# Kernel optimization log

Hardware: AMD Instinct MI355X
Metric: run time of the kernel (lower is better)

## Reference

```python
import jax, jax.numpy as jnp
import numpy as np

T, B, FEAT = 256, 512, 8
HID = 256
IN_DIM = 4  # QCNN output dim


def _linear_params(key, out_dim, in_dim, scale=0.1):
    kw, kb = jax.random.split(key)
    W = jax.random.normal(kw, (out_dim, in_dim), dtype=jnp.float32) * scale
    b = jax.random.normal(kb, (out_dim,), dtype=jnp.float32) * scale
    return W, b


def setup_inputs() -> dict:
    key = jax.random.key(0)
    ks = jax.random.split(key, 12)
    inputs = jax.random.normal(ks[0], (T, B, FEAT), dtype=jnp.float32)
    # QCNN feature extractor linears (torch Linear: W is [out, in])
    fm_w, fm_b = _linear_params(ks[1], 16, FEAT)
    c1_w, c1_b = _linear_params(ks[2], 16, 16)
    p1_w, p1_b = _linear_params(ks[3], 12, 16)
    c2_w, c2_b = _linear_params(ks[4], 8, 12)
    p2_w, p2_b = _linear_params(ks[5], 4, 8)
    c3_w, c3_b = _linear_params(ks[6], 4, 4)
    # LSTM gate linears: (IN_DIM + HID) -> HID
    f_w, f_b = _linear_params(ks[7], HID, IN_DIM + HID)
    i_w, i_b = _linear_params(ks[8], HID, IN_DIM + HID)
    u_w, u_b = _linear_params(ks[9], HID, IN_DIM + HID)
    o_w, o_b = _linear_params(ks[10], HID, IN_DIM + HID)
    # tagger head: HID -> 1
    head_w, head_b = _linear_params(ks[11], 1, HID)
    return dict(inputs=inputs, fm_w=fm_w, fm_b=fm_b, c1_w=c1_w, c1_b=c1_b,
                p1_w=p1_w, p1_b=p1_b, c2_w=c2_w, c2_b=c2_b, p2_w=p2_w, p2_b=p2_b,
                c3_w=c3_w, c3_b=c3_b, f_w=f_w, f_b=f_b, i_w=i_w, i_b=i_b,
                u_w=u_w, u_b=u_b, o_w=o_w, o_b=o_b, head_w=head_w, head_b=head_b)


def _lin(x, W, b):
    return x @ W.T + b


def reference(inputs, fm_w, fm_b, c1_w, c1_b, p1_w, p1_b, c2_w, c2_b,
              p2_w, p2_b, c3_w, c3_b, f_w, f_b, i_w, i_b, u_w, u_b,
              o_w, o_b, head_w, head_b):
    seq_len, batch, _ = inputs.shape
    # QCNN feature extractor has no cross-timestep dependency -> apply to all steps at once
    x = jnp.tanh(_lin(inputs, fm_w, fm_b))
    x = jnp.tanh(_lin(x, c1_w, c1_b))
    x = jnp.tanh(_lin(x, p1_w, p1_b))
    x = jnp.tanh(_lin(x, c2_w, c2_b))
    x = jnp.tanh(_lin(x, p2_w, p2_b))
    feats = jnp.tanh(_lin(x, c3_w, c3_b))  # [T, B, 4]

    h0 = jnp.zeros((batch, HID), dtype=inputs.dtype)
    c0 = jnp.zeros((batch, HID), dtype=inputs.dtype)

    def step(carry, xt):
        hx, cx = carry
        combined = jnp.concatenate([xt, hx], axis=1)  # [B, 4+HID]
        f = jax.nn.sigmoid(_lin(combined, f_w, f_b))
        i = jax.nn.sigmoid(_lin(combined, i_w, i_b))
        g = jnp.tanh(_lin(combined, u_w, u_b))
        o = jax.nn.sigmoid(_lin(combined, o_w, o_b))
        cx = f * cx + i * g
        hx = o * jnp.tanh(cx)
        return (hx, cx), hx

    (_, _), lstm_out = jax.lax.scan(step, (h0, c0), feats)  # [T, B, HID]
    out = _lin(lstm_out, head_w, head_b)  # [T, B, 1]
    return out
```

## Files before the change

kernel.cpp:

```cpp
#include <hip/hip_runtime.h>
#include <hip/hip_bf16.h>
#include <hip/hip_fp16.h>
#include <stdint.h>

#define T_STEPS 256
#define BATCH 512

typedef _Float16 f16x8 __attribute__((ext_vector_type(8)));
typedef _Float16 h2_t  __attribute__((ext_vector_type(2)));
typedef float    f32x4 __attribute__((ext_vector_type(4)));

__device__ __forceinline__ float fdot2(uint32_t w, uint32_t c, float acc) {
#if __has_builtin(__builtin_amdgcn_fdot2)
    h2_t a, b;
    __builtin_memcpy(&a, &w, 4);
    __builtin_memcpy(&b, &c, 4);
    return __builtin_amdgcn_fdot2(a, b, acc, false);
#else
    union { uint32_t u; _Float16 h[2]; } A, B;
    A.u = w; B.u = c;
    return acc + (float)A.h[0]*(float)B.h[0] + (float)A.h[1]*(float)B.h[1];
#endif
}

__device__ __forceinline__ float sigmoidf_(float x) {
    return 1.f / (1.f + __expf(-x));
}
__device__ __forceinline__ float tanhf_(float x) {
    float ax = fabsf(x);
    float e = __expf(-2.f * ax);
    float r = (1.f - e) / (1.f + e);
    return copysignf(r, x);
}

__device__ __forceinline__ float sel4(int d, float a, float b, float c, float e) {
    float lo = (d & 1) ? b : a;
    float hi = (d & 1) ? e : c;
    return (d & 2) ? hi : lo;
}

#define MFMA_AG(c, aa, bb) \
    asm volatile("v_mfma_f32_16x16x32_f16 %0, %1, %2, %0" : "+v"(c) : "v"(aa), "a"(bb))

__global__ void concat_qw(const float* __restrict__ fm_w, const float* __restrict__ fm_b,
                          const float* __restrict__ c1_w, const float* __restrict__ c1_b,
                          const float* __restrict__ p1_w, const float* __restrict__ p1_b,
                          const float* __restrict__ c2_w, const float* __restrict__ c2_b,
                          const float* __restrict__ p2_w, const float* __restrict__ p2_b,
                          const float* __restrict__ c3_w, const float* __restrict__ c3_b,
                          float* __restrict__ qw) {
    for (int k = threadIdx.x; k < 780; k += 256) {
        float v;
        if      (k < 128) v = fm_w[k];
        else if (k < 144) v = fm_b[k-128];
        else if (k < 400) v = c1_w[k-144];
        else if (k < 416) v = c1_b[k-400];
        else if (k < 608) v = p1_w[k-416];
        else if (k < 620) v = p1_b[k-608];
        else if (k < 716) v = c2_w[k-620];
        else if (k < 724) v = c2_b[k-716];
        else if (k < 756) v = p2_w[k-724];
        else if (k < 760) v = p2_b[k-756];
        else if (k < 776) v = c3_w[k-760];
        else              v = c3_b[k-776];
        qw[k] = v;
    }
}

__global__ void pack_bfrag(const float* __restrict__ f_w, const float* __restrict__ i_w,
                           const float* __restrict__ u_w, const float* __restrict__ o_w,
                           uint4* __restrict__ bfragsG) {
    int idx = blockIdx.x * 256 + threadIdx.x;
    int l = idx & 63, q = (idx >> 6) & 7, n = idx >> 9;
    int col = n * 16 + (l & 15);
    int g = col >> 8, j = col & 255;
    const float* W = (g == 0) ? f_w : (g == 1) ? i_w : (g == 2) ? u_w : o_w;
    union { uint4 u; _Float16 h[8]; } P;
#pragma unroll
    for (int e = 0; e < 8; ++e) {
        int k = q * 32 + ((l >> 4) * 8) + e;
        P.h[e] = (_Float16)W[j * 260 + 4 + k];
    }
    bfragsG[idx] = P.u;
}

__global__ void pack_xw(const float* __restrict__ f_w, const float* __restrict__ i_w,
                        const float* __restrict__ u_w, const float* __restrict__ o_w,
                        _Float16* __restrict__ xwG) {
    int t = blockIdx.x * 256 + threadIdx.x;
    int g = t >> 10, k = (t >> 8) & 3, j = t & 255;
    const float* W = (g == 0) ? f_w : (g == 1) ? i_w : (g == 2) ? u_w : o_w;
    xwG[t] = (_Float16)W[j * 260 + k];
}

__global__ void qcnn_kernel(const float* __restrict__ in, const float* __restrict__ qw,
                            _Float16* __restrict__ feats) {
    int r = blockIdx.x * 256 + threadIdx.x;
    const float* x = in + (size_t)r * 8;
    float v0[8];
#pragma unroll
    for (int i = 0; i < 8; ++i) v0[i] = x[i];
    float v1[16];
#pragma unroll
    for (int o = 0; o < 16; ++o) {
        float s = qw[128 + o];
#pragma unroll
        for (int i = 0; i < 8; ++i) s += qw[o*8 + i] * v0[i];
        v1[o] = tanhf_(s);
    }
    float v2[16];
#pragma unroll
    for (int o = 0; o < 16; ++o) {
        float s = qw[400 + o];
#pragma unroll
        for (int i = 0; i < 16; ++i) s += qw[144 + o*16 + i] * v1[i];
        v2[o] = tanhf_(s);
    }
    float v3[12];
#pragma unroll
    for (int o = 0; o < 12; ++o) {
        float s = qw[608 + o];
#pragma unroll
        for (int i = 0; i < 16; ++i) s += qw[416 + o*16 + i] * v2[i];
        v3[o] = tanhf_(s);
    }
    float v4[8];
#pragma unroll
    for (int o = 0; o < 8; ++o) {
        float s = qw[716 + o];
#pragma unroll
        for (int i = 0; i < 12; ++i) s += qw[620 + o*12 + i] * v3[i];
        v4[o] = tanhf_(s);
    }
    float v5[4];
#pragma unroll
    for (int o = 0; o < 4; ++o) {
        float s = qw[756 + o];
#pragma unroll
        for (int i = 0; i < 8; ++i) s += qw[724 + o*8 + i] * v4[i];
        v5[o] = tanhf_(s);
    }
    union { uint32_t u[2]; _Float16 h[4]; } P;
#pragma unroll
    for (int o = 0; o < 4; ++o) {
        float s = qw[776 + o];
#pragma unroll
        for (int i = 0; i < 4; ++i) s += qw[760 + o*4 + i] * v5[i];
        P.h[o] = (_Float16)tanhf_(s);
    }
    *reinterpret_cast<uint2*>(feats + (size_t)r * 4) = make_uint2(P.u[0], P.u[1]);
}

__global__ __launch_bounds__(256, 1)
void lstm_kernel(const uint4* __restrict__ bfragsG, const _Float16* __restrict__ xwG,
                 const _Float16* __restrict__ feats,
                 const float* __restrict__ f_b, const float* __restrict__ i_b,
                 const float* __restrict__ u_b, const float* __restrict__ o_b,
                 const float* __restrict__ head_w, const float* __restrict__ head_bp,
                 float* __restrict__ out) {
    __shared__ uint4     blds45[2][64][64];
    __shared__ uint4     blds6o[16][64];
    __shared__ __align__(16) _Float16 comb[2][2][256];
    __shared__ float     redL[2][4][2];

    const int tid = threadIdx.x;
    const int w   = tid >> 6;
    const int l   = tid & 63;
    const int d_  = l >> 4;
    const int jl  = (w * 4 + d_) * 16 + (l & 15);
    const int s0  = blockIdx.x * 2;

    for (int idx = tid; idx < 8192; idx += 256) {
        int n = idx >> 7, qq = (idx >> 6) & 1, ll = idx & 63;
        blds45[qq][n][ll] = bfragsG[(n * 8 + 4 + qq) * 64 + ll];
    }
    for (int idx = tid; idx < 1024; idx += 256) {
        int nn = idx >> 6, ll = idx & 63;
        blds6o[nn][ll] = bfragsG[((48 + nn) * 8 + 6) * 64 + ll];
    }
    reinterpret_cast<uint32_t*>(&comb[0][0][0])[tid] = 0u;

    f16x8 Br[16][4];
#pragma unroll
    for (int m = 0; m < 16; ++m) {
        const int n = (m >> 2) * 16 + w * 4 + (m & 3);
#pragma unroll
        for (int q = 0; q < 4; ++q) {
            Br[m][q] = *reinterpret_cast<const f16x8*>(bfragsG + (n * 8 + q) * 64 + l);
            asm volatile("" : "+a"(Br[m][q]));
        }
    }

    float bias_[4] = { f_b[jl], i_b[jl], u_b[jl], o_b[jl] };
    uint32_t xwp0[4], xwp1[4];
#pragma unroll
    for (int g = 0; g < 4; ++g) {
        union { uint32_t u; _Float16 h[2]; } P;
        P.h[0] = xwG[g*1024 +       jl]; P.h[1] = xwG[g*1024 + 256 + jl];
        xwp0[g] = P.u;
        P.h[0] = xwG[g*1024 + 512 + jl]; P.h[1] = xwG[g*1024 + 768 + jl];
        xwp1[g] = P.u;
    }
    const float hwj = head_w[jl];
    const float hb  = head_bp[0];
    uint2 xr0 = *reinterpret_cast<const uint2*>(feats + ((size_t)0 * BATCH + s0    ) * 4);
    uint2 xr1 = *reinterpret_cast<const uint2*>(feats + ((size_t)0 * BATCH + s0 + 1) * 4);

    __syncthreads();

    float cs0 = 0.f, cs1 = 0.f;

#pragma unroll 1
    for (int t = 0; t < T_STEPS; ++t) {
        const int cur = t & 1;
        uint2 xn0 = xr0, xn1 = xr1;
        if (t + 1 < T_STEPS) {
            xn0 = *reinterpret_cast<const uint2*>(feats + ((size_t)(t+1) * BATCH + s0    ) * 4);
            xn1 = *reinterpret_cast<const uint2*>(feats + ((size_t)(t+1) * BATCH + s0 + 1) * 4);
        }

        const _Float16* ab = &comb[cur][l & 1][(l >> 4) * 8];
        f16x8 A_[8];
#pragma unroll
        for (int q = 0; q < 8; ++q)
            A_[q] = *reinterpret_cast<const f16x8*>(ab + q * 32);

        float gv0[4], gv1[4];

#pragma unroll
        for (int g = 0; g < 4; ++g) {
            f16x8 s6[4], s7[4];
#pragma unroll
            for (int d = 0; d < 4; ++d) {
                const int n = g * 16 + w * 4 + d;
                if (g < 3) s6[d] = *reinterpret_cast<const f16x8*>(bfragsG + (n * 8 + 6) * 64 + l);
                else       s6[d] = *reinterpret_cast<const f16x8*>(&blds6o[w * 4 + d][l]);
                s7[d] = *reinterpret_cast<const f16x8*>(bfragsG + (n * 8 + 7) * 64 + l);
            }
            f16x8 b4[4], b5[4];
#pragma unroll
            for (int d = 0; d < 4; ++d) {
                const int n = g * 16 + w * 4 + d;
                b4[d] = *reinterpret_cast<const f16x8*>(&blds45[0][n][l]);
                b5[d] = *reinterpret_cast<const f16x8*>(&blds45[1][n][l]);
            }

            f32x4 c0 = {0.f,0.f,0.f,0.f}, c1 = {0.f,0.f,0.f,0.f};
            f32x4 c2 = {0.f,0.f,0.f,0.f}, c3 = {0.f,0.f,0.f,0.f};
            asm volatile("s_nop 0" : "+v"(c0), "+v"(c1), "+v"(c2), "+v"(c3));

#pragma unroll
            for (int q = 0; q < 4; ++q) {
                MFMA_AG(c0, A_[q], Br[4*g+0][q]); MFMA_AG(c1, A_[q], Br[4*g+1][q]);
                MFMA_AG(c2, A_[q], Br[4*g+2][q]); MFMA_AG(c3, A_[q], Br[4*g+3][q]);
            }
            c0 = __builtin_amdgcn_mfma_f32_16x16x32_f16(A_[4], b4[0], c0, 0, 0, 0);
            c1 = __builtin_amdgcn_mfma_f32_16x16x32_f16(A_[4], b4[1], c1, 0, 0, 0);
            c2 = __builtin_amdgcn_mfma_f32_16x16x32_f16(A_[4], b4[2], c2, 0, 0, 0);
            c3 = __builtin_amdgcn_mfma_f32_16x16x32_f16(A_[4], b4[3], c3, 0, 0, 0);
            c0 = __builtin_amdgcn_mfma_f32_16x16x32_f16(A_[5], b5[0], c0, 0, 0, 0);
            c1 = __builtin_amdgcn_mfma_f32_16x16x32_f16(A_[5], b5[1], c1, 0, 0, 0);
            c2 = __builtin_amdgcn_mfma_f32_16x16x32_f16(A_[5], b5[2], c2, 0, 0, 0);
            c3 = __builtin_amdgcn_mfma_f32_16x16x32_f16(A_[5], b5[3], c3, 0, 0, 0);
            c0 = __builtin_amdgcn_mfma_f32_16x16x32_f16(A_[6], s6[0], c0, 0, 0, 0);
            c1 = __builtin_amdgcn_mfma_f32_16x16x32_f16(A_[6], s6[1], c1, 0, 0, 0);
            c2 = __builtin_amdgcn_mfma_f32_16x16x32_f16(A_[6], s6[2], c2, 0, 0, 0);
            c3 = __builtin_amdgcn_mfma_f32_16x16x32_f16(A_[6], s6[3], c3, 0, 0, 0);
            c0 = __builtin_amdgcn_mfma_f32_16x16x32_f16(A_[7], s7[0], c0, 0, 0, 0);
            c1 = __builtin_amdgcn_mfma_f32_16x16x32_f16(A_[7], s7[1], c1, 0, 0, 0);
            c2 = __builtin_amdgcn_mfma_f32_16x16x32_f16(A_[7], s7[2], c2, 0, 0, 0);
            c3 = __builtin_amdgcn_mfma_f32_16x16x32_f16(A_[7], s7[3], c3, 0, 0, 0);

            gv0[g] = sel4(d_, c0[0], c1[0], c2[0], c3[0]);
            gv1[g] = sel4(d_, c0[1], c1[1], c2[1], c3[1]);
        }

        float pre0[4], pre1[4];
#pragma unroll
        for (int g = 0; g < 4; ++g) {
            pre0[g] = fdot2(xwp0[g], xr0.x, fdot2(xwp1[g], xr0.y, gv0[g] + bias_[g]));
            pre1[g] = fdot2(xwp0[g], xr1.x, fdot2(xwp1[g], xr1.y, gv1[g] + bias_[g]));
        }
        const float fg0 = sigmoidf_(pre0[0]), fg1 = sigmoidf_(pre1[0]);
        const float ig0 = sigmoidf_(pre0[1]), ig1 = sigmoidf_(pre1[1]);
        const float ug0 = tanhf_(pre0[2]),    ug1 = tanhf_(pre1[2]);
        const float og0 = sigmoidf_(pre0[3]), og1 = sigmoidf_(pre1[3]);
        cs0 = fg0 * cs0 + ig0 * ug0;
        cs1 = fg1 * cs1 + ig1 * ug1;
        const float h0 = og0 * tanhf_(cs0);
        const float h1 = og1 * tanhf_(cs1);

        comb[cur ^ 1][0][jl] = (_Float16)h0;
        comb[cur ^ 1][1][jl] = (_Float16)h1;

        float p0 = h0 * hwj, p1 = h1 * hwj;
#pragma unroll
        for (int off = 32; off; off >>= 1) {
            p0 += __shfl_xor(p0, off);
            p1 += __shfl_xor(p1, off);
        }
        if (l == 0) { redL[cur][w][0] = p0; redL[cur][w][1] = p1; }

        xr0 = xn0; xr1 = xn1;
        __syncthreads();

        if (tid < 2)
            out[(size_t)t * BATCH + s0 + tid] =
                (redL[cur][0][tid] + redL[cur][1][tid]) +
                (redL[cur][2][tid] + redL[cur][3][tid]) + hb;
    }
}

extern "C" void kernel_launch(void* const* d_in, const int* in_sizes, int n_in,
                              void* d_out, int out_size, void* d_ws, size_t ws_size,
                              hipStream_t stream) {
    const float* inputs = (const float*)d_in[0];
    const float* fm_w = (const float*)d_in[1];  const float* fm_b = (const float*)d_in[2];
    const float* c1_w = (const float*)d_in[3];  const float* c1_b = (const float*)d_in[4];
    const float* p1_w = (const float*)d_in[5];  const float* p1_b = (const float*)d_in[6];
    const float* c2_w = (const float*)d_in[7];  const float* c2_b = (const float*)d_in[8];
    const float* p2_w = (const float*)d_in[9];  const float* p2_b = (const float*)d_in[10];
    const float* c3_w = (const float*)d_in[11]; const float* c3_b = (const float*)d_in[12];
    const float* f_w  = (const float*)d_in[13]; const float* f_b  = (const float*)d_in[14];
    const float* i_w  = (const float*)d_in[15]; const float* i_b  = (const float*)d_in[16];
    const float* u_w  = (const float*)d_in[17]; const float* u_b  = (const float*)d_in[18];
    const float* o_w  = (const float*)d_in[19]; const float* o_b  = (const float*)d_in[20];
    const float* head_w = (const float*)d_in[21];
    const float* head_b = (const float*)d_in[22];

    uint4*     bfragsG = (uint4*)d_ws;
    _Float16*  xwG     = (_Float16*)((char*)d_ws + 524288);
    _Float16*  feats   = (_Float16*)((char*)d_ws + 532480);
    float*     qw      = (float*)((char*)d_ws + 1581056);

    hipLaunchKernelGGL(concat_qw, dim3(1), dim3(256), 0, stream,
                       fm_w, fm_b, c1_w, c1_b, p1_w, p1_b, c2_w, c2_b,
                       p2_w, p2_b, c3_w, c3_b, qw);
    hipLaunchKernelGGL(pack_bfrag, dim3(128), dim3(256), 0, stream,
                       f_w, i_w, u_w, o_w, bfragsG);
    hipLaunchKernelGGL(pack_xw, dim3(16), dim3(256), 0, stream,
                       f_w, i_w, u_w, o_w, xwG);
    hipLaunchKernelGGL(qcnn_kernel, dim3(512), dim3(256), 0, stream,
                       inputs, qw, feats);
    hipLaunchKernelGGL(lstm_kernel, dim3(256), dim3(256), 0, stream,
                       bfragsG, xwG, feats,
                       f_b, i_b, u_b, o_b, head_w, head_b, (float*)d_out);
}
```

Baseline: 635.8 us.

## Keep K-chunks 4-5 of recurrent weights in VGPRs and move chunks 6-7 to LDS

Weight fragments for K-chunks 4-5 now live in VGPRs next to the AGPR-resident chunks 0-3, and chunks 6-7 are staged fully in LDS. The per-step global/L2 reads of chunk 6-7 fragments are gone. The head-output reduction is also moved after the barrier, so each step writes the previous step's output and the final step is written after the loop. This takes one serial reduction off the critical path before the barrier, at the cost of much higher VGPR pressure and a possible spill risk.

```diff
diff --git a/kernel.cpp b/kernel.cpp
--- a/kernel.cpp
+++ b/kernel.cpp
@@ -41,6 +41,8 @@
 
 #define MFMA_AG(c, aa, bb) \
     asm volatile("v_mfma_f32_16x16x32_f16 %0, %1, %2, %0" : "+v"(c) : "v"(aa), "a"(bb))
+#define MFMA_VG(c, aa, bb) \
+    asm volatile("v_mfma_f32_16x16x32_f16 %0, %1, %2, %0" : "+v"(c) : "v"(aa), "v"(bb))
 
 __global__ void concat_qw(const float* __restrict__ fm_w, const float* __restrict__ fm_b,
                           const float* __restrict__ c1_w, const float* __restrict__ c1_b,
@@ -158,8 +160,7 @@
                  const float* __restrict__ u_b, const float* __restrict__ o_b,
                  const float* __restrict__ head_w, const float* __restrict__ head_bp,
                  float* __restrict__ out) {
-    __shared__ uint4     blds45[2][64][64];
-    __shared__ uint4     blds6o[16][64];
+    __shared__ uint4     blds67[2][64][64];
     __shared__ __align__(16) _Float16 comb[2][2][256];
     __shared__ float     redL[2][4][2];
 
@@ -172,22 +173,28 @@
 
     for (int idx = tid; idx < 8192; idx += 256) {
         int n = idx >> 7, qq = (idx >> 6) & 1, ll = idx & 63;
-        blds45[qq][n][ll] = bfragsG[(n * 8 + 4 + qq) * 64 + ll];
-    }
-    for (int idx = tid; idx < 1024; idx += 256) {
-        int nn = idx >> 6, ll = idx & 63;
-        blds6o[nn][ll] = bfragsG[((48 + nn) * 8 + 6) * 64 + ll];
+        blds67[qq][n][ll] = bfragsG[(n * 8 + 6 + qq) * 64 + ll];
     }
     reinterpret_cast<uint32_t*>(&comb[0][0][0])[tid] = 0u;
 
-    f16x8 Br[16][4];
+    f16x8 Br03[16][4];
 #pragma unroll
     for (int m = 0; m < 16; ++m) {
         const int n = (m >> 2) * 16 + w * 4 + (m & 3);
 #pragma unroll
         for (int q = 0; q < 4; ++q) {
-            Br[m][q] = *reinterpret_cast<const f16x8*>(bfragsG + (n * 8 + q) * 64 + l);
-            asm volatile("" : "+a"(Br[m][q]));
+            Br03[m][q] = *reinterpret_cast<const f16x8*>(bfragsG + (n * 8 + q) * 64 + l);
+            asm volatile("" : "+a"(Br03[m][q]));
+        }
+    }
+    f16x8 Br45[16][2];
+#pragma unroll
+    for (int m = 0; m < 16; ++m) {
+        const int n = (m >> 2) * 16 + w * 4 + (m & 3);
+#pragma unroll
+        for (int q = 0; q < 2; ++q) {
+            Br45[m][q] = *reinterpret_cast<const f16x8*>(bfragsG + (n * 8 + 4 + q) * 64 + l);
+            asm volatile("" : "+v"(Br45[m][q]));
         }
     }
 
@@ -229,20 +236,12 @@
 
 #pragma unroll
         for (int g = 0; g < 4; ++g) {
-            f16x8 s6[4], s7[4];
+            f16x8 t6[4], t7[4];
 #pragma unroll
             for (int d = 0; d < 4; ++d) {
                 const int n = g * 16 + w * 4 + d;
-                if (g < 3) s6[d] = *reinterpret_cast<const f16x8*>(bfragsG + (n * 8 + 6) * 64 + l);
-                else       s6[d] = *reinterpret_cast<const f16x8*>(&blds6o[w * 4 + d][l]);
-                s7[d] = *reinterpret_cast<const f16x8*>(bfragsG + (n * 8 + 7) * 64 + l);
-            }
-            f16x8 b4[4], b5[4];
-#pragma unroll
-            for (int d = 0; d < 4; ++d) {
-                const int n = g * 16 + w * 4 + d;
-                b4[d] = *reinterpret_cast<const f16x8*>(&blds45[0][n][l]);
-                b5[d] = *reinterpret_cast<const f16x8*>(&blds45[1][n][l]);
+                t6[d] = *reinterpret_cast<const f16x8*>(&blds67[0][n][l]);
+                t7[d] = *reinterpret_cast<const f16x8*>(&blds67[1][n][l]);
             }
 
             f32x4 c0 = {0.f,0.f,0.f,0.f}, c1 = {0.f,0.f,0.f,0.f};
@@ -251,25 +250,22 @@
 
 #pragma unroll
             for (int q = 0; q < 4; ++q) {
-                MFMA_AG(c0, A_[q], Br[4*g+0][q]); MFMA_AG(c1, A_[q], Br[4*g+1][q]);
-                MFMA_AG(c2, A_[q], Br[4*g+2][q]); MFMA_AG(c3, A_[q], Br[4*g+3][q]);
+                MFMA_AG(c0, A_[q], Br03[4*g+0][q]); MFMA_AG(c1, A_[q], Br03[4*g+1][q]);
+                MFMA_AG(c2, A_[q], Br03[4*g+2][q]); MFMA_AG(c3, A_[q], Br03[4*g+3][q]);
             }
-            c0 = __builtin_amdgcn_mfma_f32_16x16x32_f16(A_[4], b4[0], c0, 0, 0, 0);
-            c1 = __builtin_amdgcn_mfma_f32_16x16x32_f16(A_[4], b4[1], c1, 0, 0, 0);
-            c2 = __builtin_amdgcn_mfma_f32_16x16x32_f16(A_[4], b4[2], c2, 0, 0, 0);
-            c3 = __builtin_amdgcn_mfma_f32_16x16x32_f16(A_[4], b4[3], c3, 0, 0, 0);
-            c0 = __builtin_amdgcn_mfma_f32_16x16x32_f16(A_[5], b5[0], c0, 0, 0, 0);
-            c1 = __builtin_amdgcn_mfma_f32_16x16x32_f16(A_[5], b5[1], c1, 0, 0, 0);
-            c2 = __builtin_amdgcn_mfma_f32_16x16x32_f16(A_[5], b5[2], c2, 0, 0, 0);
-            c3 = __builtin_amdgcn_mfma_f32_16x16x32_f16(A_[5], b5[3], c3, 0, 0, 0);
-            c0 = __builtin_amdgcn_mfma_f32_16x16x32_f16(A_[6], s6[0], c0, 0, 0, 0);
-            c1 = __builtin_amdgcn_mfma_f32_16x16x32_f16(A_[6], s6[1], c1, 0, 0, 0);
-            c2 = __builtin_amdgcn_mfma_f32_16x16x32_f16(A_[6], s6[2], c2, 0, 0, 0);
-            c3 = __builtin_amdgcn_mfma_f32_16x16x32_f16(A_[6], s6[3], c3, 0, 0, 0);
-            c0 = __builtin_amdgcn_mfma_f32_16x16x32_f16(A_[7], s7[0], c0, 0, 0, 0);
-            c1 = __builtin_amdgcn_mfma_f32_16x16x32_f16(A_[7], s7[1], c1, 0, 0, 0);
-            c2 = __builtin_amdgcn_mfma_f32_16x16x32_f16(A_[7], s7[2], c2, 0, 0, 0);
-            c3 = __builtin_amdgcn_mfma_f32_16x16x32_f16(A_[7], s7[3], c3, 0, 0, 0);
+#pragma unroll
+            for (int q = 0; q < 2; ++q) {
+                MFMA_VG(c0, A_[4+q], Br45[4*g+0][q]); MFMA_VG(c1, A_[4+q], Br45[4*g+1][q]);
+                MFMA_VG(c2, A_[4+q], Br45[4*g+2][q]); MFMA_VG(c3, A_[4+q], Br45[4*g+3][q]);
+            }
+            c0 = __builtin_amdgcn_mfma_f32_16x16x32_f16(A_[6], t6[0], c0, 0, 0, 0);
+            c1 = __builtin_amdgcn_mfma_f32_16x16x32_f16(A_[6], t6[1], c1, 0, 0, 0);
+            c2 = __builtin_amdgcn_mfma_f32_16x16x32_f16(A_[6], t6[2], c2, 0, 0, 0);
+            c3 = __builtin_amdgcn_mfma_f32_16x16x32_f16(A_[6], t6[3], c3, 0, 0, 0);
+            c0 = __builtin_amdgcn_mfma_f32_16x16x32_f16(A_[7], t7[0], c0, 0, 0, 0);
+            c1 = __builtin_amdgcn_mfma_f32_16x16x32_f16(A_[7], t7[1], c1, 0, 0, 0);
+            c2 = __builtin_amdgcn_mfma_f32_16x16x32_f16(A_[7], t7[2], c2, 0, 0, 0);
+            c3 = __builtin_amdgcn_mfma_f32_16x16x32_f16(A_[7], t7[3], c3, 0, 0, 0);
 
             gv0[g] = sel4(d_, c0[0], c1[0], c2[0], c3[0]);
             gv1[g] = sel4(d_, c0[1], c1[1], c2[1], c3[1]);
@@ -293,6 +289,9 @@
         comb[cur ^ 1][0][jl] = (_Float16)h0;
         comb[cur ^ 1][1][jl] = (_Float16)h1;
 
+        xr0 = xn0; xr1 = xn1;
+        __syncthreads();
+
         float p0 = h0 * hwj, p1 = h1 * hwj;
 #pragma unroll
         for (int off = 32; off; off >>= 1) {
@@ -301,14 +300,17 @@
         }
         if (l == 0) { redL[cur][w][0] = p0; redL[cur][w][1] = p1; }
 
-        xr0 = xn0; xr1 = xn1;
-        __syncthreads();
-
-        if (tid < 2)
-            out[(size_t)t * BATCH + s0 + tid] =
-                (redL[cur][0][tid] + redL[cur][1][tid]) +
-                (redL[cur][2][tid] + redL[cur][3][tid]) + hb;
-    }
+        if (tid < 2 && t > 0)
+            out[(size_t)(t - 1) * BATCH + s0 + tid] =
+                (redL[cur ^ 1][0][tid] + redL[cur ^ 1][1][tid]) +
+                (redL[cur ^ 1][2][tid] + redL[cur ^ 1][3][tid]) + hb;
+    }
+
+    __syncthreads();
+    if (tid < 2)
+        out[(size_t)(T_STEPS - 1) * BATCH + s0 + tid] =
+            (redL[(T_STEPS - 1) & 1][0][tid] + redL[(T_STEPS - 1) & 1][1][tid]) +
+            (redL[(T_STEPS - 1) & 1][2][tid] + redL[(T_STEPS - 1) & 1][3][tid]) + hb;
 }
 
 extern "C" void kernel_launch(void* const* d_in, const int* in_sizes, int n_in,
```

After: 670.5 us. 1.05x slower.

## Overlap gate activations with MFMAs and defer head output past the barrier

Applied to the files above, without the earlier changes.

Computes each gate's activation immediately after its MFMA group so transcendental work overlaps with the remaining matrix ops. Moves the step barrier before the head-projection shuffle reduction and writes each output one step later, shortening the per-step critical path. Also stages more B fragments in LDS and initializes MFMA accumulators with a zero operand instead of an explicit clear. This adds LDS usage and relies on careful double-buffering of the reduction scratch.

```diff
diff --git a/kernel.cpp b/kernel.cpp
--- a/kernel.cpp
+++ b/kernel.cpp
@@ -41,6 +41,8 @@
 
 #define MFMA_AG(c, aa, bb) \
     asm volatile("v_mfma_f32_16x16x32_f16 %0, %1, %2, %0" : "+v"(c) : "v"(aa), "a"(bb))
+#define MFMA_AG0(c, aa, bb, zz) \
+    asm volatile("v_mfma_f32_16x16x32_f16 %0, %1, %2, %3" : "=&v"(c) : "v"(aa), "a"(bb), "v"(zz))
 
 __global__ void concat_qw(const float* __restrict__ fm_w, const float* __restrict__ fm_b,
                           const float* __restrict__ c1_w, const float* __restrict__ c1_b,
@@ -160,6 +162,7 @@
                  float* __restrict__ out) {
     __shared__ uint4     blds45[2][64][64];
     __shared__ uint4     blds6o[16][64];
+    __shared__ uint4     blds6b[8][64];
     __shared__ __align__(16) _Float16 comb[2][2][256];
     __shared__ float     redL[2][4][2];
 
@@ -178,6 +181,10 @@
         int nn = idx >> 6, ll = idx & 63;
         blds6o[nn][ll] = bfragsG[((48 + nn) * 8 + 6) * 64 + ll];
     }
+    for (int idx = tid; idx < 512; idx += 256) {
+        int nn = idx >> 6, ll = idx & 63;
+        blds6b[nn][ll] = bfragsG[((40 + nn) * 8 + 6) * 64 + ll];
+    }
     reinterpret_cast<uint32_t*>(&comb[0][0][0])[tid] = 0u;
 
     f16x8 Br[16][4];
@@ -205,6 +212,8 @@
     const float hb  = head_bp[0];
     uint2 xr0 = *reinterpret_cast<const uint2*>(feats + ((size_t)0 * BATCH + s0    ) * 4);
     uint2 xr1 = *reinterpret_cast<const uint2*>(feats + ((size_t)0 * BATCH + s0 + 1) * 4);
+
+    const f32x4 z4 = {0.f, 0.f, 0.f, 0.f};
 
     __syncthreads();
 
@@ -225,7 +234,7 @@
         for (int q = 0; q < 8; ++q)
             A_[q] = *reinterpret_cast<const f16x8*>(ab + q * 32);
 
-        float gv0[4], gv1[4];
+        float act0[4], act1[4];
 
 #pragma unroll
         for (int g = 0; g < 4; ++g) {
@@ -233,8 +242,9 @@
 #pragma unroll
             for (int d = 0; d < 4; ++d) {
                 const int n = g * 16 + w * 4 + d;
-                if (g < 3) s6[d] = *reinterpret_cast<const f16x8*>(bfragsG + (n * 8 + 6) * 64 + l);
-                else       s6[d] = *reinterpret_cast<const f16x8*>(&blds6o[w * 4 + d][l]);
+                if (g == 3)                 s6[d] = *reinterpret_cast<const f16x8*>(&blds6o[w * 4 + d][l]);
+                else if (g == 2 && w >= 2)  s6[d] = *reinterpret_cast<const f16x8*>(&blds6b[n - 40][l]);
+                else                        s6[d] = *reinterpret_cast<const f16x8*>(bfragsG + (n * 8 + 6) * 64 + l);
                 s7[d] = *reinterpret_cast<const f16x8*>(bfragsG + (n * 8 + 7) * 64 + l);
             }
             f16x8 b4[4], b5[4];
@@ -245,12 +255,13 @@
                 b5[d] = *reinterpret_cast<const f16x8*>(&blds45[1][n][l]);
             }
 
-            f32x4 c0 = {0.f,0.f,0.f,0.f}, c1 = {0.f,0.f,0.f,0.f};
-            f32x4 c2 = {0.f,0.f,0.f,0.f}, c3 = {0.f,0.f,0.f,0.f};
-            asm volatile("s_nop 0" : "+v"(c0), "+v"(c1), "+v"(c2), "+v"(c3));
-
-#pragma unroll
-            for (int q = 0; q < 4; ++q) {
+            f32x4 c0, c1, c2, c3;
+            MFMA_AG0(c0, A_[0], Br[4*g+0][0], z4);
+            MFMA_AG0(c1, A_[0], Br[4*g+1][0], z4);
+            MFMA_AG0(c2, A_[0], Br[4*g+2][0], z4);
+            MFMA_AG0(c3, A_[0], Br[4*g+3][0], z4);
+#pragma unroll
+            for (int q = 1; q < 4; ++q) {
                 MFMA_AG(c0, A_[q], Br[4*g+0][q]); MFMA_AG(c1, A_[q], Br[4*g+1][q]);
                 MFMA_AG(c2, A_[q], Br[4*g+2][q]); MFMA_AG(c3, A_[q], Br[4*g+3][q]);
             }
@@ -271,27 +282,24 @@
             c2 = __builtin_amdgcn_mfma_f32_16x16x32_f16(A_[7], s7[2], c2, 0, 0, 0);
             c3 = __builtin_amdgcn_mfma_f32_16x16x32_f16(A_[7], s7[3], c3, 0, 0, 0);
 
-            gv0[g] = sel4(d_, c0[0], c1[0], c2[0], c3[0]);
-            gv1[g] = sel4(d_, c0[1], c1[1], c2[1], c3[1]);
+            const float gv0 = sel4(d_, c0[0], c1[0], c2[0], c3[0]);
+            const float gv1 = sel4(d_, c0[1], c1[1], c2[1], c3[1]);
+            const float pg0 = fdot2(xwp0[g], xr0.x, fdot2(xwp1[g], xr0.y, gv0 + bias_[g]));
+            const float pg1 = fdot2(xwp0[g], xr1.x, fdot2(xwp1[g], xr1.y, gv1 + bias_[g]));
+            if (g == 2) { act0[g] = tanhf_(pg0);    act1[g] = tanhf_(pg1); }
+            else        { act0[g] = sigmoidf_(pg0); act1[g] = sigmoidf_(pg1); }
         }
 
-        float pre0[4], pre1[4];
-#pragma unroll
-        for (int g = 0; g < 4; ++g) {
-            pre0[g] = fdot2(xwp0[g], xr0.x, fdot2(xwp1[g], xr0.y, gv0[g] + bias_[g]));
-            pre1[g] = fdot2(xwp0[g], xr1.x, fdot2(xwp1[g], xr1.y, gv1[g] + bias_[g]));
-        }
-        const float fg0 = sigmoidf_(pre0[0]), fg1 = sigmoidf_(pre1[0]);
-        const float ig0 = sigmoidf_(pre0[1]), ig1 = sigmoidf_(pre1[1]);
-        const float ug0 = tanhf_(pre0[2]),    ug1 = tanhf_(pre1[2]);
-        const float og0 = sigmoidf_(pre0[3]), og1 = sigmoidf_(pre1[3]);
-        cs0 = fg0 * cs0 + ig0 * ug0;
-        cs1 = fg1 * cs1 + ig1 * ug1;
-        const float h0 = og0 * tanhf_(cs0);
-        const float h1 = og1 * tanhf_(cs1);
+        cs0 = act0[0] * cs0 + act0[1] * act0[2];
+        cs1 = act1[0] * cs1 + act1[1] * act1[2];
+        const float h0 = act0[3] * tanhf_(cs0);
+        const float h1 = act1[3] * tanhf_(cs1);
 
         comb[cur ^ 1][0][jl] = (_Float16)h0;
         comb[cur ^ 1][1][jl] = (_Float16)h1;
+
+        xr0 = xn0; xr1 = xn1;
+        __syncthreads();
 
         float p0 = h0 * hwj, p1 = h1 * hwj;
 #pragma unroll
@@ -301,14 +309,17 @@
         }
         if (l == 0) { redL[cur][w][0] = p0; redL[cur][w][1] = p1; }
 
-        xr0 = xn0; xr1 = xn1;
-        __syncthreads();
-
-        if (tid < 2)
-            out[(size_t)t * BATCH + s0 + tid] =
-                (redL[cur][0][tid] + redL[cur][1][tid]) +
-                (redL[cur][2][tid] + redL[cur][3][tid]) + hb;
-    }
+        if (tid < 2 && t > 0)
+            out[(size_t)(t - 1) * BATCH + s0 + tid] =
+                (redL[cur ^ 1][0][tid] + redL[cur ^ 1][1][tid]) +
+                (redL[cur ^ 1][2][tid] + redL[cur ^ 1][3][tid]) + hb;
+    }
+
+    __syncthreads();
+    if (tid < 2)
+        out[(size_t)(T_STEPS - 1) * BATCH + s0 + tid] =
+            (redL[(T_STEPS - 1) & 1][0][tid] + redL[(T_STEPS - 1) & 1][1][tid]) +
+            (redL[(T_STEPS - 1) & 1][2][tid] + redL[(T_STEPS - 1) & 1][3][tid]) + hb;
 }
 
 extern "C" void kernel_launch(void* const* d_in, const int* in_sizes, int n_in,
```

After: 748.3 us. 17.7% more time.
